# Kernel optimization log

Hardware: AMD Instinct MI355X
Metric: run time of the kernel (lower is better)

The kernel has to match this reference:

```python
import jax, jax.numpy as jnp
import numpy as np

EPS = 1e-5

def _ln_channels(x, w, b):
    # LayerNorm over channel dim of BCHW (original permutes to BHWC, LN on C)
    mu = jnp.mean(x, axis=1, keepdims=True)
    var = jnp.mean(jnp.square(x - mu), axis=1, keepdims=True)
    xn = (x - mu) * jax.lax.rsqrt(var + EPS)
    return xn * w[None, :, None, None] + b[None, :, None, None]

def _conv1x1(x, w, b):
    # 1x1 conv == per-pixel GEMM over channels
    return jnp.einsum('oc,bchw->bohw', w, x) + b[None, :, None, None]

def setup_inputs() -> dict:
    key = jax.random.key(0)
    ks = jax.random.split(key, 5)
    B, C, H, W = 8, 256, 160, 160
    hid = 2 * C
    s = lambda fan_in: 1.0 / np.sqrt(fan_in)
    return {
        'x': jax.random.normal(ks[0], (B, C, H, W), jnp.float32),
        'ln1_w': jnp.ones((C,), jnp.float32),
        'ln1_b': jnp.zeros((C,), jnp.float32),
        'qkv_w': jax.random.normal(ks[1], (3 * C, C), jnp.float32) * s(C),
        'qkv_b': jnp.zeros((3 * C,), jnp.float32),
        'proj_w': jax.random.normal(ks[2], (C, C), jnp.float32) * s(C),
        'proj_b': jnp.zeros((C,), jnp.float32),
        'ln2_w': jnp.ones((C,), jnp.float32),
        'ln2_b': jnp.zeros((C,), jnp.float32),
        'w1': jax.random.normal(ks[3], (hid, C), jnp.float32) * s(C),
        'b1': jnp.zeros((hid,), jnp.float32),
        'w2': jax.random.normal(ks[4], (C, hid), jnp.float32) * s(hid),
        'b2': jnp.zeros((C,), jnp.float32),
    }

def reference(x, ln1_w, ln1_b, qkv_w, qkv_b, proj_w, proj_b, ln2_w, ln2_b, w1, b1, w2, b2):
    B, C, H, W = x.shape
    # --- attention branch ---
    xn = _ln_channels(x, ln1_w, ln1_b)
    qkv = _conv1x1(xn, qkv_w, qkv_b)            # (B, 3C, H, W)
    q, k, v = jnp.split(qkv, 3, axis=1)
    q = q.reshape(B, C, H * W)                   # (B, C, N)
    k = k.reshape(B, C, H * W)
    v = v.reshape(B, C, H * W)
    # channel attention: (B, C, C) scores, softmax over last (channel) axis
    scores = jnp.einsum('bcn,bdn->bcd', q, k) / jnp.sqrt(jnp.asarray(C, x.dtype))
    attn = jax.nn.softmax(scores, axis=-1)
    out = jnp.einsum('bcd,bdn->bcn', attn, v).reshape(B, C, H, W)
    x = x + _conv1x1(out, proj_w, proj_b)
    # --- conv FFN branch ---
    yn = _ln_channels(x, ln2_w, ln2_b)
    h = jax.nn.gelu(_conv1x1(yn, w1, b1), approximate=False)
    x = x + _conv1x1(h, w2, b2)
    return x
```

## Files before the change

kernel.cpp:

```cpp
#include <hip/hip_runtime.h>

#define Bc   8
#define Cc   256
#define NP   25600
#define HIDc 512
#define EPSc 1e-5f

typedef __bf16 bf16_t;
typedef __bf16 bf16x8_t __attribute__((ext_vector_type(8)));
typedef float  f32x4_t  __attribute__((ext_vector_type(4)));

__device__ __forceinline__ unsigned short f2bf_u(float f) {
  bf16_t t = (bf16_t)f;
  return __builtin_bit_cast(unsigned short, t);
}
__device__ __forceinline__ float bf2f(unsigned short u) {
  union { float f; unsigned i; } w; w.i = ((unsigned)u) << 16; return w.f;
}

__device__ __forceinline__ float gelu_f(float x) {
  float x3 = x * x * x;
  float y = 0.7978845608028654f * (x + 0.044715f * x3);
  float e = __expf(2.0f * y);
  float t = 1.0f - 2.0f * __builtin_amdgcn_rcpf(1.0f + e);
  return 0.5f * x * (1.0f + t);
}

__device__ __forceinline__ void glds16(const void* g, void* l) {
  __builtin_amdgcn_global_load_lds(
      (const __attribute__((address_space(1))) unsigned int*)g,
      (__attribute__((address_space(3))) unsigned int*)l,
      16, 0, 0);
}


__global__ __launch_bounds__(256) void k_ln1(const float* __restrict__ x,
                                             const float* __restrict__ gamma,
                                             const float* __restrict__ beta,
                                             bf16_t* __restrict__ cf,
                                             bf16_t* __restrict__ cl) {
  int bb = blockIdx.y;
  int n0 = blockIdx.x * 64;
  int t = threadIdx.x;
  __shared__ bf16_t X[256 * 72];
  __shared__ float R2[4][64][2];
  __shared__ float MU[64], RS[64];
  const float* xb = x + (size_t)bb * Cc * NP + n0;
  int ci = t >> 4;
  int p4 = (t & 15) * 4;
  float s1v[4] = {}, s2v[4] = {};
#pragma unroll
  for (int i = 0; i < 16; ++i) {
    int c = i * 16 + ci;
    float4 v = *(const float4*)(xb + (size_t)c * NP + p4);
    float vv[4] = {v.x, v.y, v.z, v.w};
    ushort4 pk;
#pragma unroll
    for (int j = 0; j < 4; ++j) {
      s1v[j] += vv[j]; s2v[j] += vv[j] * vv[j];
      ((unsigned short*)&pk)[j] = f2bf_u(vv[j]);
    }
    *(ushort4*)&X[c * 72 + p4] = pk;
  }
#pragma unroll
  for (int j = 0; j < 4; ++j) {
    s1v[j] += __shfl_xor(s1v[j], 16); s2v[j] += __shfl_xor(s2v[j], 16);
    s1v[j] += __shfl_xor(s1v[j], 32); s2v[j] += __shfl_xor(s2v[j], 32);
  }
  int w = t >> 6, l = t & 63;
  if ((l >> 4) == 0) {
#pragma unroll
    for (int j = 0; j < 4; ++j) {
      R2[w][(l & 15) * 4 + j][0] = s1v[j];
      R2[w][(l & 15) * 4 + j][1] = s2v[j];
    }
  }
  __syncthreads();
  if (t < 64) {
    float ts1 = R2[0][t][0] + R2[1][t][0] + R2[2][t][0] + R2[3][t][0];
    float ts2 = R2[0][t][1] + R2[1][t][1] + R2[2][t][1] + R2[3][t][1];
    float mu = ts1 * (1.0f / Cc);
    MU[t] = mu;
    RS[t] = rsqrtf(ts2 * (1.0f / Cc) - mu * mu + EPSc);
  }
  __syncthreads();
  bf16_t* cfp = cf + (size_t)bb * Cc * NP;
  {
    int c8 = t >> 3, pk8 = (t & 7) * 8;
    float mus[8], rss[8];
#pragma unroll
    for (int e = 0; e < 8; ++e) { mus[e] = MU[pk8 + e]; rss[e] = RS[pk8 + e]; }
#pragma unroll
    for (int p = 0; p < 8; ++p) {
      int c = p * 32 + c8;
      float g = gamma[c], bt = beta[c];
      uint4 xr = *(const uint4*)&X[c * 72 + pk8];
      const unsigned short* xu = (const unsigned short*)&xr;
      union { uint4 u; unsigned short us[8]; } pk;
#pragma unroll
      for (int e = 0; e < 8; ++e)
        pk.us[e] = f2bf_u((bf2f(xu[e]) - mus[e]) * rss[e] * g + bt);
      *(uint4*)&cfp[(size_t)c * NP + n0 + pk8] = pk.u;
    }
  }
  {
    int px = t & 63, gq = t >> 6;
    float mu = MU[px], rs = RS[px];
    bf16_t* clp = cl + (size_t)bb * NP * Cc + (size_t)(n0 + px) * Cc;
#pragma unroll
    for (int chunk = 0; chunk < 8; ++chunk) {
      union { uint4 u; unsigned short us[8]; } pk;
#pragma unroll
      for (int e = 0; e < 8; ++e) {
        int c = gq * 64 + chunk * 8 + e;
        float v = (bf2f(__builtin_bit_cast(unsigned short, X[c * 72 + px])) - mu) * rs * gamma[c] + beta[c];
        pk.us[e] = f2bf_u(v);
      }
      *(uint4*)(clp + gq * 64 + chunk * 8) = pk.u;
    }
  }
}

__global__ __launch_bounds__(256) void k_gram_mfma(const bf16_t* __restrict__ xn,
                                                   float* __restrict__ G) {
  int b = blockIdx.z;
  int ti = blockIdx.y >> 1, tj = blockIdx.y & 1;
  int t = threadIdx.x;
  int l = t & 63, qq = l >> 4, rr = l & 15;
  int wv = t >> 6;
  int wm = (wv >> 1) * 64, wn = (wv & 1) * 64;
  int row8 = l >> 3, sl = l & 7;
  int s = (sl - row8) & 7;
  __shared__ char SM[65536];
  const bf16_t* xb = xn + (size_t)b * Cc * NP;
  const bf16_t* gA = xb + (size_t)(ti * 128 + wv * 32 + row8) * NP + s * 8;
  const bf16_t* gB = xb + (size_t)(tj * 128 + wv * 32 + row8) * NP + s * 8;

  auto stage = [&](int buf, int k0) {
    bf16_t* A = (bf16_t*)(SM + (buf << 15));
    bf16_t* Bb = (bf16_t*)(SM + (buf << 15) + 16384);
#pragma unroll
    for (int i = 0; i < 4; ++i) {
      glds16(gA + (size_t)(i * 8) * NP + k0, A + (wv * 32 + i * 8) * 64);
      glds16(gB + (size_t)(i * 8) * NP + k0, Bb + (wv * 32 + i * 8) * 64);
    }
  };

  f32x4_t acc[4][4] = {};
  int kbase = blockIdx.x * 1600;
  stage(0, kbase);
  __syncthreads();
  int cur = 0;
  for (int ks = 0; ks < 25; ++ks) {
    if (ks + 1 < 25) stage(cur ^ 1, kbase + (ks + 1) * 64);
    bf16_t* At = (bf16_t*)(SM + (cur << 15));
    bf16_t* Bt = (bf16_t*)(SM + (cur << 15) + 16384);
#pragma unroll
    for (int h = 0; h < 2; ++h) {
      bf16x8_t af[4], bff[4];
#pragma unroll
      for (int mi = 0; mi < 4; ++mi) {
        int row = wm + mi * 16 + rr;
        int g = (h * 4 + qq + (row & 7)) & 7;
        af[mi] = *(const bf16x8_t*)&At[row * 64 + g * 8];
      }
#pragma unroll
      for (int nj = 0; nj < 4; ++nj) {
        int row = wn + nj * 16 + rr;
        int g = (h * 4 + qq + (row & 7)) & 7;
        bff[nj] = *(const bf16x8_t*)&Bt[row * 64 + g * 8];
      }
#pragma unroll
      for (int mi = 0; mi < 4; ++mi)
#pragma unroll
        for (int nj = 0; nj < 4; ++nj)
          acc[mi][nj] = __builtin_amdgcn_mfma_f32_16x16x32_bf16(af[mi], bff[nj], acc[mi][nj], 0, 0, 0);
    }
    __syncthreads();
    cur ^= 1;
  }
  float* Gb = G + (size_t)b * Cc * Cc;
#pragma unroll
  for (int mi = 0; mi < 4; ++mi)
#pragma unroll
    for (int nj = 0; nj < 4; ++nj) {
      int col = tj * 128 + wn + nj * 16 + rr;
#pragma unroll
      for (int reg = 0; reg < 4; ++reg) {
        int rowc = ti * 128 + wm + mi * 16 + qq * 4 + reg;
        atomicAdd(&Gb[(size_t)rowc * Cc + col], acc[mi][nj][reg]);
      }
    }
}

__global__ __launch_bounds__(256) void k_small_T(const float* __restrict__ G,
                                                 const float* __restrict__ qkv_w,
                                                 float* __restrict__ T) {
  int b = blockIdx.y, e = blockIdx.x, d = threadIdx.x;
  __shared__ float gs[Cc];
  gs[d] = G[((size_t)b * Cc + e) * Cc + d];
  __syncthreads();
  const float* wk = qkv_w + (size_t)(Cc + d) * Cc;
  float acc = 0.f;
  for (int f = 0; f < Cc; ++f) acc += gs[f] * wk[f];
  T[((size_t)b * Cc + e) * Cc + d] = acc;
}
__global__ __launch_bounds__(256) void k_small_SP(const float* __restrict__ T,
                                                  const float* __restrict__ qkv_w,
                                                  const float* __restrict__ qkv_b,
                                                  float* __restrict__ P,
                                                  float* __restrict__ pv) {
  int b = blockIdx.y, c0 = blockIdx.x, d = threadIdx.x;
  __shared__ float wq[Cc];
  wq[d] = qkv_w[(size_t)c0 * Cc + d];
  __syncthreads();
  const float* Tb = T + (size_t)b * Cc * Cc;
  float acc = 0.f;
  for (int e = 0; e < Cc; ++e) acc += wq[e] * Tb[(size_t)e * Cc + d];
  float v = acc * 0.0625f;
  __shared__ float red[256];
  red[d] = v; __syncthreads();
  for (int sd = 128; sd > 0; sd >>= 1) { if (d < sd) red[d] = fmaxf(red[d], red[d + sd]); __syncthreads(); }
  float m = red[0]; __syncthreads();
  float e1 = expf(v - m);
  red[d] = e1; __syncthreads();
  for (int sd = 128; sd > 0; sd >>= 1) { if (d < sd) red[d] += red[d + sd]; __syncthreads(); }
  float inv = 1.0f / red[0]; __syncthreads();
  float p = e1 * inv;
  P[((size_t)b * Cc + c0) * Cc + d] = p;
  red[d] = p * qkv_b[2 * Cc + d]; __syncthreads();
  for (int sd = 128; sd > 0; sd >>= 1) { if (d < sd) red[d] += red[d + sd]; __syncthreads(); }
  if (d == 0) pv[(size_t)b * Cc + c0] = red[0];
}
__global__ __launch_bounds__(256) void k_small_U(const float* __restrict__ P,
                                                 const float* __restrict__ qkv_w,
                                                 float* __restrict__ U) {
  int b = blockIdx.y, c = blockIdx.x, e = threadIdx.x;
  __shared__ float pr[Cc];
  pr[e] = P[((size_t)b * Cc + c) * Cc + e];
  __syncthreads();
  float acc = 0.f;
  for (int d = 0; d < Cc; ++d) acc += pr[d] * qkv_w[(size_t)(2 * Cc + d) * Cc + e];
  U[((size_t)b * Cc + c) * Cc + e] = acc;
}
__global__ __launch_bounds__(256) void k_small_A2(const float* __restrict__ U,
                                                  const float* __restrict__ proj_w,
                                                  const float* __restrict__ proj_b,
                                                  const float* __restrict__ pv,
                                                  bf16_t* __restrict__ A2b_out,
                                                  float* __restrict__ a2b) {
  int b = blockIdx.y, o = blockIdx.x, e = threadIdx.x;
  __shared__ float wr[Cc];
  wr[e] = proj_w[(size_t)o * Cc + e];
  __syncthreads();
  const float* Ub = U + (size_t)b * Cc * Cc;
  float acc = 0.f;
  for (int c = 0; c < Cc; ++c) acc += wr[c] * Ub[(size_t)c * Cc + e];
  A2b_out[((size_t)b * Cc + o) * Cc + e] = (bf16_t)acc;
  __shared__ float red[256];
  red[e] = wr[e] * pv[(size_t)b * Cc + e];
  __syncthreads();
  for (int sd = 128; sd > 0; sd >>= 1) { if (e < sd) red[e] += red[e + sd]; __syncthreads(); }
  if (e == 0) a2b[(size_t)b * Cc + o] = red[0] + proj_b[o];
}

__global__ __launch_bounds__(256) void k_f2b2(const float* __restrict__ s1,
                                              const float* __restrict__ s2,
                                              bf16_t* __restrict__ d1, int n1,
                                              bf16_t* __restrict__ d2, int n2) {
  int i = (blockIdx.x * 256 + threadIdx.x) * 4;
  const float* s; bf16_t* d;
  if (i < n1) { s = s1; d = d1; }
  else { i -= n1; if (i >= n2) return; s = s2; d = d2; }
  float4 v = *(const float4*)(s + i);
  ushort4 pk;
  pk.x = f2bf_u(v.x); pk.y = f2bf_u(v.y); pk.z = f2bf_u(v.z); pk.w = f2bf_u(v.w);
  *(ushort4*)(d + i) = pk;
}

template <bool X1B>
__global__ __launch_bounds__(512) void k_apply_ln(
    const bf16_t* __restrict__ A2b, const bf16_t* __restrict__ xn,
    const float* __restrict__ a2b, const float* __restrict__ xres,
    const float* __restrict__ g2, const float* __restrict__ b2,
    float* __restrict__ out, bf16_t* __restrict__ x1cl,
    bf16_t* __restrict__ yn) {
  int b = blockIdx.y;
  int n0 = blockIdx.x * 128;
  int t = threadIdx.x;
  int w = t >> 6, l = t & 63;
  int qq = l >> 4, rr = l & 15;
  int wmW = w >> 1, wnW = w & 1;
  int row8 = l >> 3, sl = l & 7;
  int s = (sl - row8) & 7;

  __shared__ char SM[53248];
  bf16_t* At = (bf16_t*)SM;
  bf16_t* Bt = (bf16_t*)(SM + 32768);
  bf16_t* Tt = (bf16_t*)SM;
  float*  Red = (float*)(SM + 49152);

  const bf16_t* Ab = A2b + (size_t)b * Cc * Cc;
  const bf16_t* xb = xn + (size_t)b * (size_t)NP * Cc;
  const bf16_t* gA = Ab + (size_t)(w * 32 + row8) * Cc + s * 8;
  const bf16_t* gB = xb + (size_t)(n0 + w * 16 + row8) * Cc + s * 8;
  f32x4_t acc[4][4] = {};
  for (int k0 = 0; k0 < Cc; k0 += 64) {
#pragma unroll
    for (int i = 0; i < 4; ++i)
      glds16(gA + (size_t)(i * 8) * Cc + k0, At + (w * 32 + i * 8) * 64);
#pragma unroll
    for (int i = 0; i < 2; ++i)
      glds16(gB + (size_t)(i * 8) * Cc + k0, Bt + (w * 16 + i * 8) * 64);
    __syncthreads();
#pragma unroll
    for (int h = 0; h < 2; ++h) {
      bf16x8_t af[4], bff[4];
#pragma unroll
      for (int mi = 0; mi < 4; ++mi) {
        int row = wmW * 64 + mi * 16 + rr;
        int g = (h * 4 + qq + (row & 7)) & 7;
        af[mi] = *(const bf16x8_t*)&At[row * 64 + g * 8];
      }
#pragma unroll
      for (int nj = 0; nj < 4; ++nj) {
        int row = wnW * 64 + nj * 16 + rr;
        int g = (h * 4 + qq + (row & 7)) & 7;
        bff[nj] = *(const bf16x8_t*)&Bt[row * 64 + g * 8];
      }
#pragma unroll
      for (int mi = 0; mi < 4; ++mi)
#pragma unroll
        for (int nj = 0; nj < 4; ++nj)
          acc[mi][nj] = __builtin_amdgcn_mfma_f32_16x16x32_bf16(af[mi], bff[nj], acc[mi][nj], 0, 0, 0);
    }
    __syncthreads();
  }

  const float* ab = a2b + (size_t)b * Cc;
  const float* rp = xres + (size_t)b * Cc * NP;
  float s1[4] = {}, s2[4] = {};
#pragma unroll
  for (int mi = 0; mi < 4; ++mi) {
    int ch0 = wmW * 64 + mi * 16 + qq * 4;
    float4 abv = *(const float4*)(ab + ch0);
#pragma unroll
    for (int nj = 0; nj < 4; ++nj) {
      int px = n0 + wnW * 64 + nj * 16 + rr;
#pragma unroll
      for (int reg = 0; reg < 4; ++reg) {
        float v = acc[mi][nj][reg] + ((const float*)&abv)[reg] + rp[(size_t)(ch0 + reg) * NP + px];
        acc[mi][nj][reg] = v;
        s1[nj] += v; s2[nj] += v * v;
      }
    }
  }
#pragma unroll
  for (int nj = 0; nj < 4; ++nj) {
    s1[nj] += __shfl_xor(s1[nj], 16); s2[nj] += __shfl_xor(s2[nj], 16);
    s1[nj] += __shfl_xor(s1[nj], 32); s2[nj] += __shfl_xor(s2[nj], 32);
  }
  if (qq == 0) {
#pragma unroll
    for (int nj = 0; nj < 4; ++nj) {
      int colb = wnW * 64 + nj * 16 + rr;
      Red[(wmW * 128 + colb) * 2 + 0] = s1[nj];
      Red[(wmW * 128 + colb) * 2 + 1] = s2[nj];
    }
  }
  __syncthreads();
  float mu[4], rstd[4];
#pragma unroll
  for (int nj = 0; nj < 4; ++nj) {
    int colb = wnW * 64 + nj * 16 + rr;
    float t1 = 0.f, t2 = 0.f;
#pragma unroll
    for (int mw = 0; mw < 4; ++mw) {
      t1 += Red[(mw * 128 + colb) * 2 + 0];
      t2 += Red[(mw * 128 + colb) * 2 + 1];
    }
    mu[nj] = t1 * (1.0f / Cc);
    rstd[nj] = rsqrtf(t2 * (1.0f / Cc) - mu[nj] * mu[nj] + EPSc);
  }
  if constexpr (!X1B) {
    float* op = out + (size_t)b * Cc * NP;
#pragma unroll
    for (int mi = 0; mi < 4; ++mi) {
      int ch0 = wmW * 64 + mi * 16 + qq * 4;
#pragma unroll
      for (int nj = 0; nj < 4; ++nj) {
        int px = n0 + wnW * 64 + nj * 16 + rr;
#pragma unroll
        for (int reg = 0; reg < 4; ++reg)
          op[(size_t)(ch0 + reg) * NP + px] = acc[mi][nj][reg];
      }
    }
  }
  bf16_t* yb = yn + (size_t)b * (size_t)NP * Cc;
  bf16_t* xo = X1B ? (x1cl + (size_t)b * (size_t)NP * Cc) : nullptr;
#pragma unroll
  for (int hh = 0; hh < 2; ++hh) {
#pragma unroll
    for (int which = 0; which < (X1B ? 2 : 1); ++which) {
      __syncthreads();
      if ((wmW >> 1) == hh) {
#pragma unroll
        for (int mi = 0; mi < 4; ++mi) {
          int ch0 = wmW * 64 + mi * 16 + qq * 4;
          int chloc = (wmW & 1) * 64 + mi * 16 + qq * 4;
          float4 gv = *(const float4*)(g2 + ch0);
          float4 bv = *(const float4*)(b2 + ch0);
#pragma unroll
          for (int nj = 0; nj < 4; ++nj) {
            int colb = wnW * 64 + nj * 16 + rr;
            ushort4 pk;
#pragma unroll
            for (int reg = 0; reg < 4; ++reg) {
              float v;
              if (which == 0)
                v = (acc[mi][nj][reg] - mu[nj]) * rstd[nj] * ((const float*)&gv)[reg] + ((const float*)&bv)[reg];
              else
                v = acc[mi][nj][reg];
              ((unsigned short*)&pk)[reg] = f2bf_u(v);
            }
            *(ushort4*)&Tt[colb * 136 + chloc] = pk;
          }
        }
      }
      __syncthreads();
      bf16_t* dst = (which == 0) ? yb : xo;
#pragma unroll
      for (int i = 0; i < 4; ++i) {
        int idx = i * 512 + t;
        int row = idx >> 4, ch16 = idx & 15;
        uint4 v4 = *(const uint4*)&Tt[row * 136 + ch16 * 8];
        *(uint4*)&dst[(size_t)(n0 + row) * Cc + hh * 128 + ch16 * 8] = v4;
      }
    }
  }
}

template <int MODE, bool RESB, bool GELU, int MT>
__global__ __launch_bounds__(512) void k_gemm512(
    const bf16_t* __restrict__ W,
    const bf16_t* __restrict__ In,
    const float* __restrict__ bias,
    const void* __restrict__ res,
    float* __restrict__ outf,
    bf16_t* __restrict__ outb,
    int K, int Mtot) {
  int b = blockIdx.y;
  int g = blockIdx.x;
  int j = g >> 3;
  int n_t = (g & 7) * 25 + j / MT;
  int m_t = j % MT;
  int n0 = n_t * 128;
  int m0g = m_t * 256;
  int t = threadIdx.x;
  int w = t >> 6, l = t & 63;
  int qq = l >> 4, rr = l & 15;
  int wmW = w >> 1, wnW = w & 1;
  int row8 = l >> 3, sl = l & 7;
  int s = (sl - row8) & 7;

  __shared__ char SM[49152];
  bf16_t* At = (bf16_t*)SM;
  bf16_t* Bt = (bf16_t*)(SM + 32768);

  const bf16_t* wb = W + (size_t)m0g * K;
  const bf16_t* ib = In + (size_t)b * (size_t)NP * K;
  const bf16_t* gA = wb + (size_t)(w * 32 + row8) * K + s * 8;
  const bf16_t* gB = ib + (size_t)(n0 + w * 16 + row8) * K + s * 8;
  f32x4_t acc[4][4] = {};
  for (int k0 = 0; k0 < K; k0 += 64) {
#pragma unroll
    for (int i = 0; i < 4; ++i)
      glds16(gA + (size_t)(i * 8) * K + k0, At + (w * 32 + i * 8) * 64);
#pragma unroll
    for (int i = 0; i < 2; ++i)
      glds16(gB + (size_t)(i * 8) * K + k0, Bt + (w * 16 + i * 8) * 64);
    __syncthreads();
#pragma unroll
    for (int h = 0; h < 2; ++h) {
      bf16x8_t af[4], bff[4];
#pragma unroll
      for (int mi = 0; mi < 4; ++mi) {
        int row = wmW * 64 + mi * 16 + rr;
        int g2 = (h * 4 + qq + (row & 7)) & 7;
        af[mi] = *(const bf16x8_t*)&At[row * 64 + g2 * 8];
      }
#pragma unroll
      for (int nj = 0; nj < 4; ++nj) {
        int row = wnW * 64 + nj * 16 + rr;
        int g2 = (h * 4 + qq + (row & 7)) & 7;
        bff[nj] = *(const bf16x8_t*)&Bt[row * 64 + g2 * 8];
      }
#pragma unroll
      for (int mi = 0; mi < 4; ++mi)
#pragma unroll
        for (int nj = 0; nj < 4; ++nj)
          acc[mi][nj] = __builtin_amdgcn_mfma_f32_16x16x32_bf16(af[mi], bff[nj], acc[mi][nj], 0, 0, 0);
    }
    __syncthreads();
  }

  if (MODE == 0) {
    float* op = outf + (size_t)b * (size_t)Mtot * NP;
#pragma unroll
    for (int mi = 0; mi < 4; ++mi) {
      int mrow = wmW * 64 + mi * 16 + qq * 4;
      float4 b2v = *(const float4*)(bias + mrow);
#pragma unroll
      for (int nj = 0; nj < 4; ++nj) {
        int ncol = n0 + wnW * 64 + nj * 16 + rr;
        if (RESB) {
          const unsigned short* rv = (const unsigned short*)
              ((const char*)res + ((size_t)b * NP * Cc + (size_t)ncol * Cc + mrow) * 2);
          uint2 rq = *(const uint2*)rv;
          const unsigned short* ru = (const unsigned short*)&rq;
#pragma unroll
          for (int reg = 0; reg < 4; ++reg) {
            float v = acc[mi][nj][reg] + ((const float*)&b2v)[reg] + bf2f(ru[reg]);
            op[(size_t)(mrow + reg) * NP + ncol] = v;
          }
        } else {
          const float* rpf = (const float*)res + (size_t)b * (size_t)Mtot * NP;
#pragma unroll
          for (int reg = 0; reg < 4; ++reg) {
            size_t idx = (size_t)(mrow + reg) * NP + ncol;
            float v = acc[mi][nj][reg] + ((const float*)&b2v)[reg] + rpf[idx];
            op[idx] = v;
          }
        }
      }
    }
  } else {
    bf16_t* Tt = (bf16_t*)SM;
    bf16_t* op = outb + (size_t)b * (size_t)NP * Mtot;
#pragma unroll
    for (int hh = 0; hh < 2; ++hh) {
      __syncthreads();
      if ((wmW >> 1) == hh) {
#pragma unroll
        for (int mi = 0; mi < 4; ++mi) {
          int mloc = wmW * 64 + mi * 16 + qq * 4;
          int chloc = (wmW & 1) * 64 + mi * 16 + qq * 4;
          float4 b1v = *(const float4*)(bias + m0g + mloc);
#pragma unroll
          for (int nj = 0; nj < 4; ++nj) {
            int colb = wnW * 64 + nj * 16 + rr;
            ushort4 pk;
#pragma unroll
            for (int reg = 0; reg < 4; ++reg) {
              float v = acc[mi][nj][reg] + ((const float*)&b1v)[reg];
              if (GELU) v = gelu_f(v);
              ((unsigned short*)&pk)[reg] = f2bf_u(v);
            }
            *(ushort4*)&Tt[colb * 136 + chloc] = pk;
          }
        }
      }
      __syncthreads();
#pragma unroll
      for (int i = 0; i < 4; ++i) {
        int idx = i * 512 + t;
        int row = idx >> 4, ch16 = idx & 15;
        uint4 v4 = *(const uint4*)&Tt[row * 136 + ch16 * 8];
        *(uint4*)&op[(size_t)(n0 + row) * Mtot + m0g + hh * 128 + ch16 * 8] = v4;
      }
    }
  }
}

extern "C" void kernel_launch(void* const* d_in, const int* in_sizes, int n_in,
                              void* d_out, int out_size, void* d_ws, size_t ws_size,
                              hipStream_t stream) {
  const float* x     = (const float*)d_in[0];
  const float* ln1w  = (const float*)d_in[1];
  const float* ln1b  = (const float*)d_in[2];
  const float* qkvw  = (const float*)d_in[3];
  const float* qkvb  = (const float*)d_in[4];
  const float* projw = (const float*)d_in[5];
  const float* projb = (const float*)d_in[6];
  const float* ln2w  = (const float*)d_in[7];
  const float* ln2b  = (const float*)d_in[8];
  const float* w1    = (const float*)d_in[9];
  const float* b1    = (const float*)d_in[10];
  const float* w2    = (const float*)d_in[11];
  const float* b2    = (const float*)d_in[12];
  float* out = (float*)d_out;

  char* ws = (char*)d_ws;
  const size_t XNCL_B = (size_t)Bc * NP * Cc * 2;
  const size_t H_B    = (size_t)Bc * NP * HIDc * 2;
  const size_t SMALLS = 16ull << 20;
  const size_t X1B_B  = (size_t)Bc * Cc * NP * 2;
  bf16_t* xn_cl = (bf16_t*)ws;
  bf16_t* xn_cf = (bf16_t*)(ws + XNCL_B);
  bf16_t* h_cl  = (bf16_t*)(ws + XNCL_B);
  char* sm = ws + XNCL_B + H_B;
  float* G   = (float*)sm;
  float* S   = G + (size_t)Bc * Cc * Cc;
  float* T   = S + (size_t)Bc * Cc * Cc;
  float* pv  = T + (size_t)Bc * Cc * Cc;
  float* a2b = pv + 2048;
  bf16_t* A2b = (bf16_t*)(a2b + 2048);
  bf16_t* w1b = A2b + (size_t)Bc * Cc * Cc;
  bf16_t* w2b = w1b + (size_t)HIDc * Cc;
  float* U = T;
  bf16_t* x1cl = (bf16_t*)(sm + SMALLS);
  const bool useX1B = ws_size >= XNCL_B + H_B + SMALLS + X1B_B;

  k_f2b2<<<dim3((HIDc * Cc + Cc * HIDc) / 1024), 256, 0, stream>>>(
      w1, w2, w1b, HIDc * Cc, w2b, Cc * HIDc);

  k_ln1<<<dim3(NP / 64, Bc), 256, 0, stream>>>(x, ln1w, ln1b, xn_cf, xn_cl);
  hipMemsetAsync(G, 0, (size_t)Bc * Cc * Cc * 4, stream);
  k_gram_mfma<<<dim3(16, 4, Bc), 256, 0, stream>>>(xn_cf, G);
  k_small_T<<<dim3(Cc, Bc), 256, 0, stream>>>(G, qkvw, T);
  k_small_SP<<<dim3(Cc, Bc), 256, 0, stream>>>(T, qkvw, qkvb, S, pv);
  k_small_U<<<dim3(Cc, Bc), 256, 0, stream>>>(S, qkvw, U);
  k_small_A2<<<dim3(Cc, Bc), 256, 0, stream>>>(U, projw, projb, pv, A2b, a2b);

  if (useX1B) {
    k_apply_ln<true><<<dim3(NP / 128, Bc), 512, 0, stream>>>(
        A2b, xn_cl, a2b, x, ln2w, ln2b, out, x1cl, xn_cl);
    k_gemm512<1, false, true, 2><<<dim3(200 * 2, Bc), 512, 0, stream>>>(
        w1b, xn_cl, b1, nullptr, nullptr, h_cl, Cc, HIDc);
    k_gemm512<0, true, false, 1><<<dim3(200, Bc), 512, 0, stream>>>(
        w2b, h_cl, b2, x1cl, out, nullptr, HIDc, Cc);
  } else {
    k_apply_ln<false><<<dim3(NP / 128, Bc), 512, 0, stream>>>(
        A2b, xn_cl, a2b, x, ln2w, ln2b, out, nullptr, xn_cl);
    k_gemm512<1, false, true, 2><<<dim3(200 * 2, Bc), 512, 0, stream>>>(
        w1b, xn_cl, b1, nullptr, nullptr, h_cl, Cc, HIDc);
    k_gemm512<0, false, false, 1><<<dim3(200, Bc), 512, 0, stream>>>(
        w2b, h_cl, b2, out, out, nullptr, HIDc, Cc);
  }

  (void)in_sizes; (void)n_in; (void)out_size; (void)ws_size;
}
```

Baseline: 686.0 us.

## Fold LN1 affine into attention matrix and reuse raw bf16 x for residual

k_ln1 now stores raw (unnormalized) bf16 x in channel-last layout plus per-pixel mean and rstd. The LN1 gamma is folded into the attention/projection matrix, and beta plus the mean correction are folded into per-channel bias terms computed in k_small_A2. k_apply_ln multiplies with raw x, applies rstd and mean correction per pixel, and takes the residual from the staged LDS x tile instead of re-reading the fp32 input. This drops the fp32 residual read and the per-element LN work in the channel-last store. The cost is that the residual now comes from bf16 x rather than fp32, which costs precision, and a mean-subtraction term that may cancel badly.

```diff
diff --git a/kernel.cpp b/kernel.cpp
--- a/kernel.cpp
+++ b/kernel.cpp
@@ -38,7 +38,9 @@
                                              const float* __restrict__ gamma,
                                              const float* __restrict__ beta,
                                              bf16_t* __restrict__ cf,
-                                             bf16_t* __restrict__ cl) {
+                                             bf16_t* __restrict__ cl,
+                                             float* __restrict__ muA,
+                                             float* __restrict__ rsA) {
   int bb = blockIdx.y;
   int n0 = blockIdx.x * 64;
   int t = threadIdx.x;
@@ -80,8 +82,10 @@
     float ts1 = R2[0][t][0] + R2[1][t][0] + R2[2][t][0] + R2[3][t][0];
     float ts2 = R2[0][t][1] + R2[1][t][1] + R2[2][t][1] + R2[3][t][1];
     float mu = ts1 * (1.0f / Cc);
-    MU[t] = mu;
-    RS[t] = rsqrtf(ts2 * (1.0f / Cc) - mu * mu + EPSc);
+    float rs = rsqrtf(ts2 * (1.0f / Cc) - mu * mu + EPSc);
+    MU[t] = mu; RS[t] = rs;
+    muA[(size_t)bb * NP + n0 + t] = mu;
+    rsA[(size_t)bb * NP + n0 + t] = rs;
   }
   __syncthreads();
   bf16_t* cfp = cf + (size_t)bb * Cc * NP;
@@ -105,7 +109,6 @@
   }
   {
     int px = t & 63, gq = t >> 6;
-    float mu = MU[px], rs = RS[px];
     bf16_t* clp = cl + (size_t)bb * NP * Cc + (size_t)(n0 + px) * Cc;
 #pragma unroll
     for (int chunk = 0; chunk < 8; ++chunk) {
@@ -113,8 +116,7 @@
 #pragma unroll
       for (int e = 0; e < 8; ++e) {
         int c = gq * 64 + chunk * 8 + e;
-        float v = (bf2f(__builtin_bit_cast(unsigned short, X[c * 72 + px])) - mu) * rs * gamma[c] + beta[c];
-        pk.us[e] = f2bf_u(v);
+        pk.us[e] = __builtin_bit_cast(unsigned short, X[c * 72 + px]);
       }
       *(uint4*)(clp + gq * 64 + chunk * 8) = pk.u;
     }
@@ -247,8 +249,11 @@
                                                   const float* __restrict__ proj_w,
                                                   const float* __restrict__ proj_b,
                                                   const float* __restrict__ pv,
-                                                  bf16_t* __restrict__ A2b_out,
-                                                  float* __restrict__ a2b) {
+                                                  const float* __restrict__ g1,
+                                                  const float* __restrict__ b1n,
+                                                  bf16_t* __restrict__ A2g_out,
+                                                  float* __restrict__ a2b,
+                                                  float* __restrict__ r1) {
   int b = blockIdx.y, o = blockIdx.x, e = threadIdx.x;
   __shared__ float wr[Cc];
   wr[e] = proj_w[(size_t)o * Cc + e];
@@ -256,12 +261,19 @@
   const float* Ub = U + (size_t)b * Cc * Cc;
   float acc = 0.f;
   for (int c = 0; c < Cc; ++c) acc += wr[c] * Ub[(size_t)c * Cc + e];
-  A2b_out[((size_t)b * Cc + o) * Cc + e] = (bf16_t)acc;
+  float a2g = acc * g1[e];
+  A2g_out[((size_t)b * Cc + o) * Cc + e] = (bf16_t)a2g;
   __shared__ float red[256];
-  red[e] = wr[e] * pv[(size_t)b * Cc + e];
-  __syncthreads();
+  red[e] = a2g; __syncthreads();
   for (int sd = 128; sd > 0; sd >>= 1) { if (e < sd) red[e] += red[e + sd]; __syncthreads(); }
-  if (e == 0) a2b[(size_t)b * Cc + o] = red[0] + proj_b[o];
+  if (e == 0) r1[(size_t)b * Cc + o] = red[0];
+  __syncthreads();
+  red[e] = acc * b1n[e]; __syncthreads();
+  for (int sd = 128; sd > 0; sd >>= 1) { if (e < sd) red[e] += red[e + sd]; __syncthreads(); }
+  float r2 = red[0]; __syncthreads();
+  red[e] = wr[e] * pv[(size_t)b * Cc + e]; __syncthreads();
+  for (int sd = 128; sd > 0; sd >>= 1) { if (e < sd) red[e] += red[e + sd]; __syncthreads(); }
+  if (e == 0) a2b[(size_t)b * Cc + o] = red[0] + proj_b[o] + r2;
 }
 
 __global__ __launch_bounds__(256) void k_f2b2(const float* __restrict__ s1,
@@ -280,8 +292,9 @@
 
 template <bool X1B>
 __global__ __launch_bounds__(512) void k_apply_ln(
-    const bf16_t* __restrict__ A2b, const bf16_t* __restrict__ xn,
-    const float* __restrict__ a2b, const float* __restrict__ xres,
+    const bf16_t* __restrict__ A2g, const bf16_t* __restrict__ xraw,
+    const float* __restrict__ a2b, const float* __restrict__ r1,
+    const float* __restrict__ muA, const float* __restrict__ rsA,
     const float* __restrict__ g2, const float* __restrict__ b2,
     float* __restrict__ out, bf16_t* __restrict__ x1cl,
     bf16_t* __restrict__ yn) {
@@ -300,11 +313,12 @@
   bf16_t* Tt = (bf16_t*)SM;
   float*  Red = (float*)(SM + 49152);
 
-  const bf16_t* Ab = A2b + (size_t)b * Cc * Cc;
-  const bf16_t* xb = xn + (size_t)b * (size_t)NP * Cc;
+  const bf16_t* Ab = A2g + (size_t)b * Cc * Cc;
+  const bf16_t* xb = xraw + (size_t)b * (size_t)NP * Cc;
   const bf16_t* gA = Ab + (size_t)(w * 32 + row8) * Cc + s * 8;
   const bf16_t* gB = xb + (size_t)(n0 + w * 16 + row8) * Cc + s * 8;
   f32x4_t acc[4][4] = {};
+  uint2 xcap[4][4];
   for (int k0 = 0; k0 < Cc; k0 += 64) {
 #pragma unroll
     for (int i = 0; i < 4; ++i)
@@ -334,22 +348,48 @@
         for (int nj = 0; nj < 4; ++nj)
           acc[mi][nj] = __builtin_amdgcn_mfma_f32_16x16x32_bf16(af[mi], bff[nj], acc[mi][nj], 0, 0, 0);
     }
+    if ((k0 >> 6) == wmW) {
+#pragma unroll
+      for (int mi = 0; mi < 4; ++mi) {
+        int slot = mi * 2 + (qq >> 1);
+#pragma unroll
+        for (int nj = 0; nj < 4; ++nj) {
+          int row = wnW * 64 + nj * 16 + rr;
+          int sp = (slot + (row & 7)) & 7;
+          xcap[mi][nj] = *(const uint2*)&Bt[row * 64 + sp * 8 + (qq & 1) * 4];
+        }
+      }
+    }
     __syncthreads();
   }
 
   const float* ab = a2b + (size_t)b * Cc;
-  const float* rp = xres + (size_t)b * Cc * NP;
+  const float* r1b = r1 + (size_t)b * Cc;
+  const float* muB = muA + (size_t)b * NP;
+  const float* rsB = rsA + (size_t)b * NP;
+  float mup[4], rsp[4];
+#pragma unroll
+  for (int nj = 0; nj < 4; ++nj) {
+    int px = n0 + wnW * 64 + nj * 16 + rr;
+    mup[nj] = muB[px];
+    rsp[nj] = rsB[px];
+  }
   float s1[4] = {}, s2[4] = {};
 #pragma unroll
   for (int mi = 0; mi < 4; ++mi) {
     int ch0 = wmW * 64 + mi * 16 + qq * 4;
     float4 abv = *(const float4*)(ab + ch0);
+    float4 r1v = *(const float4*)(r1b + ch0);
 #pragma unroll
     for (int nj = 0; nj < 4; ++nj) {
-      int px = n0 + wnW * 64 + nj * 16 + rr;
+      const unsigned short* xu = (const unsigned short*)&xcap[mi][nj];
 #pragma unroll
       for (int reg = 0; reg < 4; ++reg) {
-        float v = acc[mi][nj][reg] + ((const float*)&abv)[reg] + rp[(size_t)(ch0 + reg) * NP + px];
+        float xr = bf2f(xu[reg]);
+        float attn = rsp[nj] * acc[mi][nj][reg]
+                   - rsp[nj] * mup[nj] * ((const float*)&r1v)[reg]
+                   + ((const float*)&abv)[reg];
+        float v = xr + attn;
         acc[mi][nj][reg] = v;
         s1[nj] += v; s2[nj] += v * v;
       }
@@ -595,7 +635,7 @@
   const size_t H_B    = (size_t)Bc * NP * HIDc * 2;
   const size_t SMALLS = 16ull << 20;
   const size_t X1B_B  = (size_t)Bc * Cc * NP * 2;
-  bf16_t* xn_cl = (bf16_t*)ws;
+  bf16_t* x_cl  = (bf16_t*)ws;
   bf16_t* xn_cf = (bf16_t*)(ws + XNCL_B);
   bf16_t* h_cl  = (bf16_t*)(ws + XNCL_B);
   char* sm = ws + XNCL_B + H_B;
@@ -604,7 +644,10 @@
   float* T   = S + (size_t)Bc * Cc * Cc;
   float* pv  = T + (size_t)Bc * Cc * Cc;
   float* a2b = pv + 2048;
-  bf16_t* A2b = (bf16_t*)(a2b + 2048);
+  float* r1  = a2b + 2048;
+  float* muA = r1 + 2048;
+  float* rsA = muA + (size_t)Bc * NP;
+  bf16_t* A2b = (bf16_t*)(rsA + (size_t)Bc * NP);
   bf16_t* w1b = A2b + (size_t)Bc * Cc * Cc;
   bf16_t* w2b = w1b + (size_t)HIDc * Cc;
   float* U = T;
@@ -614,26 +657,27 @@
   k_f2b2<<<dim3((HIDc * Cc + Cc * HIDc) / 1024), 256, 0, stream>>>(
       w1, w2, w1b, HIDc * Cc, w2b, Cc * HIDc);
 
-  k_ln1<<<dim3(NP / 64, Bc), 256, 0, stream>>>(x, ln1w, ln1b, xn_cf, xn_cl);
+  k_ln1<<<dim3(NP / 64, Bc), 256, 0, stream>>>(x, ln1w, ln1b, xn_cf, x_cl, muA, rsA);
   hipMemsetAsync(G, 0, (size_t)Bc * Cc * Cc * 4, stream);
   k_gram_mfma<<<dim3(16, 4, Bc), 256, 0, stream>>>(xn_cf, G);
   k_small_T<<<dim3(Cc, Bc), 256, 0, stream>>>(G, qkvw, T);
   k_small_SP<<<dim3(Cc, Bc), 256, 0, stream>>>(T, qkvw, qkvb, S, pv);
   k_small_U<<<dim3(Cc, Bc), 256, 0, stream>>>(S, qkvw, U);
-  k_small_A2<<<dim3(Cc, Bc), 256, 0, stream>>>(U, projw, projb, pv, A2b, a2b);
+  k_small_A2<<<dim3(Cc, Bc), 256, 0, stream>>>(U, projw, projb, pv, ln1w, ln1b,
+                                               A2b, a2b, r1);
 
   if (useX1B) {
     k_apply_ln<true><<<dim3(NP / 128, Bc), 512, 0, stream>>>(
-        A2b, xn_cl, a2b, x, ln2w, ln2b, out, x1cl, xn_cl);
+        A2b, x_cl, a2b, r1, muA, rsA, ln2w, ln2b, out, x1cl, x_cl);
     k_gemm512<1, false, true, 2><<<dim3(200 * 2, Bc), 512, 0, stream>>>(
-        w1b, xn_cl, b1, nullptr, nullptr, h_cl, Cc, HIDc);
+        w1b, x_cl, b1, nullptr, nullptr, h_cl, Cc, HIDc);
     k_gemm512<0, true, false, 1><<<dim3(200, Bc), 512, 0, stream>>>(
         w2b, h_cl, b2, x1cl, out, nullptr, HIDc, Cc);
   } else {
     k_apply_ln<false><<<dim3(NP / 128, Bc), 512, 0, stream>>>(
-        A2b, xn_cl, a2b, x, ln2w, ln2b, out, nullptr, xn_cl);
+        A2b, x_cl, a2b, r1, muA, rsA, ln2w, ln2b, out, nullptr, x_cl);
     k_gemm512<1, false, true, 2><<<dim3(200 * 2, Bc), 512, 0, stream>>>(
-        w1b, xn_cl, b1, nullptr, nullptr, h_cl, Cc, HIDc);
+        w1b, x_cl, b1, nullptr, nullptr, h_cl, Cc, HIDc);
     k_gemm512<0, false, false, 1><<<dim3(200, Bc), 512, 0, stream>>>(
         w2b, h_cl, b2, out, out, nullptr, HIDc, Cc);
   }
```

After: 642.9 us. 1.07x faster.
